# Kernel optimization log

Measured on AMD Instinct MI355X. Metric: run time of the kernel, lower is better.

## Reference

```python
import jax, jax.numpy as jnp
from jax import lax
import numpy as np
from functools import partial

B, C, H, W = 4, 3, 256, 256
HW = H * W
KCAP = 32          # max tracked components per (batch, class) slot
MAX_ITER = 5
KSIZE = 5


def _depthwise_sum(x, k):
    c = x.shape[1]
    w = jnp.ones((c, 1, k, k), x.dtype)
    return lax.conv_general_dilated(x, w, (1, 1), [(k // 2, k // 2)] * 2,
                                    feature_group_count=c,
                                    dimension_numbers=('NCHW', 'OIHW', 'NCHW'))


def erode(x):
    return (_depthwise_sum(x, KSIZE) >= KSIZE * KSIZE - 0.5).astype(x.dtype)


def dilate(x):
    return (_depthwise_sum(x, KSIZE) > 0.5).astype(x.dtype)


def _maxpool3_int(L):
    return lax.reduce_window(L, jnp.int32(0), lax.max, (1, 1, 3, 3), (1, 1, 1, 1),
                             [(0, 0), (0, 0), (1, 1), (1, 1)])


def label_cc(binary):
    # connected-component labeling by iterated 3x3 max-pool of pixel indices,
    # exactly as find_components_max_pool (labels = max flat pixel index in comp)
    b = lax.stop_gradient(binary) > 0.5
    idx = jnp.arange(HW, dtype=jnp.int32).reshape(1, 1, H, W)
    L0 = jnp.where(b, idx, 0)

    def cond(st):
        return st[1]

    def body(st):
        L, _ = st
        Ln = jnp.where(b, _maxpool3_int(L), 0)
        return Ln, jnp.any(Ln != L)

    L, _ = lax.while_loop(cond, body, (L0, jnp.array(True)))
    return L


def extract_components(Lf, binf):
    # per (b,c): top-KCAP components sorted by comp.sum() = size*label/maxL (desc)
    flat = Lf.reshape(-1)
    sizes = jnp.zeros((HW,), jnp.float32).at[flat].add(binf.reshape(-1))
    idx = jnp.arange(HW, dtype=jnp.int32)
    is_root = (flat == idx) & (flat > 0)  # label 0 excluded, as in torch code
    key = jnp.where(is_root, lax.stop_gradient(sizes) * idx.astype(jnp.float32), -1.0)
    _, top_lab = lax.top_k(key, KCAP)
    valid = key[top_lab] > 0.0
    maxL = jnp.maximum(flat.max(), 1).astype(jnp.float32)
    v = top_lab.astype(jnp.float32)
    s = jnp.where(valid, sizes[top_lab] * v / maxL, 0.0)  # comp.sum()
    lab = jnp.where(valid, top_lab, -1)
    # component tensor = mask * label/maxL, exactly mask*L/max(L) of the original
    comps = (Lf[None] == lab[:, None, None]).astype(jnp.float32) * (v / maxL)[:, None, None]
    return s, comps, valid


def process_step(P, n, bar, s, comps, valid, t):
    # overlaps vs components stored BEFORE this step; new comps within a step
    # are pixel-disjoint so they can never match each other (overlap == 0).
    OV = jnp.einsum('jhw,khw->jk', comps, P)

    def body(carry, inp):
        P, n, bar = carry
        s_j, comp_j, valid_j, ov_j = inp
        best = jnp.argmax(ov_j)
        matched = ov_j[best] > 0.0
        widx = jnp.clip(jnp.where(matched, best, n), 0, KCAP - 1)
        can = valid_j & (matched | (n < KCAP))
        bar = bar.at[widx, t].set(jnp.where(can, s_j, bar[widx, t]))
        add = valid_j & (~matched) & (n < KCAP)
        nw = jnp.minimum(n, KCAP - 1)
        P = P.at[nw].set(jnp.where(add, comp_j, P[nw]))
        return (P, n + add.astype(n.dtype), bar), None

    (P, n, bar), _ = lax.scan(body, (P, n, bar), (s, comps, valid, OV))
    return P, n, bar


def compute_barcodes(binary):
    half = MAX_ITER // 2
    seq = [(binary, half)]
    m = binary
    for t in range(half):
        m = erode(m)
        seq.append((m, half + t + 1))
    m = binary
    for t in range(half):
        m = dilate(m)
        seq.append((m, half - t - 1))
    BC = B * C
    P = jnp.zeros((BC, KCAP, H, W), jnp.float32)
    n = jnp.zeros((BC,), jnp.int32)
    bar = jnp.zeros((BC, KCAP, MAX_ITER), jnp.float32)
    for mp, t in seq:  # fixed 5-step schedule (structural loop)
        L = label_cc(mp).reshape(BC, H, W)
        s, comps, valid = jax.vmap(extract_components)(L, mp.reshape(BC, H, W))
        P, n, bar = jax.vmap(partial(process_step, t=t))(P, n, bar, s, comps, valid)
    return bar.reshape(B, C, KCAP, MAX_ITER), n.reshape(B, C)


def topo_forward(predictions, gumbel, targets):
    y_soft = jax.nn.softmax(predictions + gumbel, axis=1)
    hard = jax.nn.one_hot(jnp.argmax(y_soft, axis=1), C, axis=1, dtype=jnp.float32)
    binary_pred = hard + y_soft - lax.stop_gradient(y_soft)  # straight-through
    binary_tgt = jnp.moveaxis(jax.nn.one_hot(targets, C, dtype=jnp.float32), -1, 1)
    bp, n_p = compute_barcodes(binary_pred)
    bt, n_t = compute_barcodes(binary_tgt)
    k = jnp.arange(KCAP)
    valid_p = k[None, None] < n_p[:, :, None]
    has_t = k[None, None] < n_t[:, :, None]
    pmax = bp.max(-1)
    pmax = jnp.where(pmax > 0, pmax, 1.0)
    tgt = jnp.where(has_t[..., None], bt, 0.0)
    term = jnp.sum((tgt - bp) ** 2, -1) / pmax ** 2
    losses = jnp.sum(jnp.where(valid_p, term, 0.0), axis=(1, 2))
    return losses.mean()  # reduction='mean'


def setup_inputs() -> dict:
    key = jax.random.key(0)
    k1, k2, k3 = jax.random.split(key, 3)
    # blob-like logits: low-res noise upsampled so component counts stay < KCAP
    lo = jax.random.normal(k1, (B, C, 16, 16), jnp.float32)
    predictions = 8.0 * jax.image.resize(lo, (B, C, H, W), 'linear')
    lo_t = jax.random.normal(k2, (B, C, 16, 16), jnp.float32)
    targets = jnp.argmax(jax.image.resize(lo_t, (B, C, H, W), 'linear'), axis=1).astype(jnp.int32)
    u = jax.random.uniform(k3, (B, C, H, W), jnp.float32, minval=1e-6, maxval=1.0 - 1e-6)
    gumbel = -jnp.log(-jnp.log(u))  # standard Gumbel noise (F.gumbel_softmax)
    return {"predictions": predictions, "gumbel": gumbel, "targets": targets}


def reference(predictions, gumbel, targets):
    return topo_forward(predictions, gumbel, targets)
```

## Files before the change

### kernel.cpp

```cpp
#include <hip/hip_runtime.h>

#define NB 4
#define NC 3
#define BC 12
#define HW 65536
#define KCAP 32
#define MAXI 5
#define RUNCAP 16384
#define NSLOT 120
#define NCH 24

typedef unsigned long long u64;
typedef unsigned int u32;

__device__ __forceinline__ int uf_find(int* P, int x){
  while (true){
    int p = P[x];
    if (p == x) return x;
    int gp = P[p];
    if (gp == p) return p;
    P[x] = gp;
    x = gp;
  }
}
__device__ __forceinline__ void uf_union_max(int* P, int a, int b){
  while (true){
    a = uf_find(P, a); b = uf_find(P, b);
    if (a == b) return;
    if (a > b){ int t = a; a = b; b = t; }
    int old = atomicCAS(&P[a], a, b);
    if (old == a) return;
    a = old;
  }
}

template<typename F>
__device__ __forceinline__ void walk_runs(const u64* wv, F&& emit){
  int open_s = -1;
  #pragma unroll
  for (int wi = 0; wi < 4; wi++){
    u64 v = wv[wi];
    int base = wi << 6;
    int pos = 0;
    while (pos < 64){
      u64 rem = v >> pos;
      if (open_s >= 0){
        u64 nz = ~rem;
        int z = nz ? __builtin_ctzll(nz) : 64;
        if (z >= 64 - pos){ pos = 64; }
        else { emit(open_s, base + pos + z); open_s = -1; pos += z; }
      } else {
        if (rem == 0ull){ pos = 64; }
        else {
          int o = __builtin_ctzll(rem);
          open_s = base + pos + o;
          pos += o;
        }
      }
    }
  }
  if (open_s >= 0) emit(open_s, 256);
}

__global__ void k_bin(const float* __restrict__ pred, const float* __restrict__ gum,
                      const int* __restrict__ tgt, u64* __restrict__ bmAll){
  int g = blockIdx.x * 256 + threadIdx.x;
  int b = g >> 16, p = g & (HW - 1);
  size_t base = (size_t)b * NC * HW + p;
  float v0 = pred[base]        + gum[base];
  float v1 = pred[base + HW]   + gum[base + HW];
  float v2 = pred[base + 2*HW] + gum[base + 2*HW];
  int a = 0; float m = v0;
  if (v1 > m){ m = v1; a = 1; }
  if (v2 > m){ m = v2; a = 2; }
  int tg = tgt[(size_t)b * HW + p];
  u64 p0 = __ballot(a == 0), p1 = __ballot(a == 1), p2 = __ballot(a == 2);
  u64 t0 = __ballot(tg == 0), t1 = __ballot(tg == 1), t2 = __ballot(tg == 2);
  if ((threadIdx.x & 63) == 0){
    int w = p >> 6;
    int sp = b * NC;
    bmAll[(size_t)(sp + 0) * 1024 + w] = p0;
    bmAll[(size_t)(sp + 1) * 1024 + w] = p1;
    bmAll[(size_t)(sp + 2) * 1024 + w] = p2;
    int st = 60 + b * NC;
    bmAll[(size_t)(st + 0) * 1024 + w] = t0;
    bmAll[(size_t)(st + 1) * 1024 + w] = t1;
    bmAll[(size_t)(st + 2) * 1024 + w] = t2;
  }
}

__global__ void k_morph4(const u64* __restrict__ bmAll, u64* __restrict__ bmAllW,
                         int4 srcs, int4 dsts, int4 flgs){
  int t = blockIdx.x * 256 + threadIdx.x;
  int job = t / 12288, rest = t % 12288;
  int s = rest >> 10, word = rest & 1023;
  int row = word >> 2, w = word & 3;
  int srcG = job == 0 ? srcs.x : job == 1 ? srcs.y : job == 2 ? srcs.z : srcs.w;
  int dstG = job == 0 ? dsts.x : job == 1 ? dsts.y : job == 2 ? dsts.z : dsts.w;
  int er   = job == 0 ? flgs.x : job == 1 ? flgs.y : job == 2 ? flgs.z : flgs.w;
  const u64* bs = bmAll + (size_t)(srcG * BC + s) * 1024;
  u64 res = er ? ~0ull : 0ull;
  for (int dy = -2; dy <= 2; dy++){
    int y = row + dy;
    if (y < 0 || y > 255){ if (er) res = 0; continue; }
    const u64* rw = bs + y * 4;
    u64 m = rw[w];
    u64 l = (w > 0) ? rw[w-1] : 0ull;
    u64 r = (w < 3) ? rw[w+1] : 0ull;
    u64 x1l = (m << 1) | (l >> 63);
    u64 x2l = (m << 2) | (l >> 62);
    u64 x1r = (m >> 1) | (r << 63);
    u64 x2r = (m >> 2) | (r << 62);
    u64 h = er ? (m & x1l & x2l & x1r & x2r) : (m | x1l | x2l | x1r | x2r);
    res = er ? (res & h) : (res | h);
  }
  bmAllW[(size_t)(dstG * BC + s) * 1024 + word] = res;
}

__global__ __launch_bounds__(1024) void k_cc_runs(
    const u64* __restrict__ bmAll, u32* __restrict__ selRuns,
    int* __restrict__ selCnt, float* __restrict__ sSel, float* __restrict__ scaleSel){
  __shared__ int par[RUNCAP];
  __shared__ u32 pkz[RUNCAP];
  __shared__ int rs[257];
  __shared__ u64 wcand[16*KCAP];
  __shared__ u64 selKeys[KCAP];
  __shared__ int selRoot[KCAP];
  __shared__ int wsum[4], wsum2[4];
  __shared__ int lmS;
  int u = blockIdx.x, t = threadIdx.x;
  int lane = t & 63, wid = t >> 6;
  bool rowT = t < 256;
  u64 wv[4] = {0,0,0,0};
  int nr = 0;
  if (rowT){
    const u64* bp = bmAll + (size_t)u * 1024 + t * 4;
    #pragma unroll
    for (int i = 0; i < 4; i++) wv[i] = bp[i];
    walk_runs(wv, [&](int a, int b){ (void)a; (void)b; nr++; });
  }
  if (t == 0) lmS = 0;
  {
    int v = nr;
    #pragma unroll
    for (int d = 1; d < 64; d <<= 1){
      int o = __shfl_up(v, d);
      if (lane >= d) v += o;
    }
    if (rowT && lane == 63) wsum[wid] = v;
    __syncthreads();
    if (rowT){
      int pre = 0;
      for (int q = 0; q < wid; q++) pre += wsum[q];
      rs[t] = pre + v - nr;
      if (t == 255) rs[256] = pre + v;
    }
    __syncthreads();
  }
  int NR = rs[256];
  int NRc = NR < RUNCAP ? NR : RUNCAP;
  int myBase = rowT ? rs[t] : 0;
  for (int i = t; i < NRc; i += 1024) par[i] = i;
  if (rowT){
    int o = myBase;
    walk_runs(wv, [&](int a, int b){
      if (o < RUNCAP) pkz[o] = ((u32)t << 16) | ((u32)a << 8) | (u32)(b - 1);
      o++;
    });
  }
  __syncthreads();
  for (int i = t; i < NRc; i += 1024){
    u32 v = pkz[i];
    int r = v >> 16;
    if (r == 0) continue;
    int s2 = (int)((v >> 8) & 255), E2 = (int)(v & 255);
    int a0 = rs[r-1], a1 = rs[r];
    if (a1 > NRc) a1 = NRc;
    if (a0 >= a1) continue;
    int lo = a0, hi = a1;
    while (lo < hi){
      int mid = (lo + hi) >> 1;
      if ((int)(pkz[mid] & 255) >= s2 - 1) hi = mid; else lo = mid + 1;
    }
    for (int j = lo; j < a1; j++){
      int s1 = (int)((pkz[j] >> 8) & 255);
      if (s1 > E2 + 1) break;
      uf_union_max(par, i, j);
    }
  }
  __syncthreads();
  for (int i = t; i < NRc; i += 1024){
    int r = i, p = par[r];
    while (p != r){ r = p; p = par[r]; }
    par[i] = r;
  }
  __syncthreads();
  {
    int lm = 0;
    for (int i0 = 0; i0 < NRc; i0 += 1024){
      int i = i0 + t;
      int root = -1, len = 0;
      if (i < NRc){
        u32 v = pkz[i];
        int s0 = (int)((v >> 8) & 255), E = (int)(v & 255);
        len = E - s0 + 1;
        root = par[i] & 16383;
        lm = max(lm, (int)(v >> 16) * 256 + E);
      }
      int val = len;
      int prev = __shfl_up(root, 1);
      unsigned flg = (lane == 0 || prev != root) ? 1u : 0u;
      #pragma unroll
      for (int d = 1; d < 64; d <<= 1){
        int ov = __shfl_up(val, d);
        unsigned of = __shfl_up(flg, d);
        if (lane >= d){
          if (!flg) val += ov;
          flg |= of;
        }
      }
      int nroot = __shfl_down(root, 1);
      bool last = (lane == 63) || (nroot != root);
      if (i < NRc && last) atomicAdd(&par[root], val << 14);
    }
    #pragma unroll
    for (int off = 32; off > 0; off >>= 1) lm = max(lm, __shfl_xor(lm, off));
    if (lane == 0) atomicMax(&lmS, lm);
  }
  __syncthreads();
  float maxLf = (float)(lmS >= 1 ? lmS : 1);
  for (int i = t; i < NRc; i += 1024){
    int pv = par[i];
    if ((pv & 16383) == i){
      u32 v = pkz[i];
      int lab = (int)(v >> 16) * 256 + (int)(v & 255);
      if (lab > 0){
        float key = (float)((u32)pv >> 14) * (float)lab;
        pkz[i] = __float_as_uint(key);
        par[i] = (lab << 14) | i;
      } else {
        pkz[i] = 0;
      }
    }
  }
  __syncthreads();
  {
    u64 myBest = 0;
    for (int i = t; i < NRc; i += 1024){
      int pv = par[i];
      if ((pv & 16383) != i) continue;
      u32 kh = pkz[i];
      if (!kh) continue;
      u64 cand = ((u64)kh << 32) | ((u64)(0xFFFFu - ((u32)pv >> 14)) << 16) | (u64)i;
      if (cand > myBest) myBest = cand;
    }
    if (lane < KCAP) wcand[wid*KCAP + lane] = 0;
    for (int r = 0; r < KCAP; r++){
      u64 b = myBest;
      #pragma unroll
      for (int off = 32; off > 0; off >>= 1){
        u64 o = __shfl_xor(b, off);
        b = (o > b) ? o : b;
      }
      if (b == 0) break;
      if (lane == 0) wcand[wid*KCAP + r] = b;
      if (myBest == b){
        pkz[(int)(b & 16383)] = 0;
        myBest = 0;
        for (int i = t; i < NRc; i += 1024){
          int pv = par[i];
          if ((pv & 16383) != i) continue;
          u32 kh = pkz[i];
          if (!kh) continue;
          u64 cand = ((u64)kh << 32) | ((u64)(0xFFFFu - ((u32)pv >> 14)) << 16) | (u64)i;
          if (cand > myBest) myBest = cand;
        }
      }
    }
  }
  __syncthreads();
  if (wid == 0){
    u64 c[8];
    #pragma unroll
    for (int q = 0; q < 8; q++) c[q] = wcand[q*64 + lane];
    if (lane < KCAP) selKeys[lane] = 0;
    for (int r = 0; r < KCAP; r++){
      u64 b = 0;
      #pragma unroll
      for (int q = 0; q < 8; q++) b = (c[q] > b) ? c[q] : b;
      #pragma unroll
      for (int off = 32; off > 0; off >>= 1){
        u64 o = __shfl_xor(b, off);
        b = (o > b) ? o : b;
      }
      if (b == 0) break;
      #pragma unroll
      for (int q = 0; q < 8; q++) if (c[q] == b) c[q] = 0;
      if (lane == 0) selKeys[r] = b;
    }
  }
  __syncthreads();
  if (t < KCAP){
    u64 k = selKeys[t];
    if (k){
      int lab = 0xFFFF - (int)((k >> 16) & 0xFFFF);
      selRoot[t] = (int)(k & 0x3FFF);
      sSel[u*KCAP + t]     = __uint_as_float((u32)(k >> 32)) / maxLf;
      scaleSel[u*KCAP + t] = (float)lab / maxLf;
    } else {
      selRoot[t] = -1;
      sSel[u*KCAP + t] = 0.0f;
      scaleSel[u*KCAP + t] = 0.0f;
    }
  }
  __syncthreads();
  for (int i = t; i < NRc; i += 1024) pkz[i] = 255u;
  __syncthreads();
  if (t < KCAP && selRoot[t] >= 0) pkz[selRoot[t]] = (u32)t;
  __syncthreads();
  int c = 0;
  if (rowT){
    int o = myBase;
    walk_runs(wv, [&](int a, int b){
      if (o < RUNCAP && pkz[par[o] & 16383] < KCAP) c++;
      o++;
    });
  }
  {
    int v = c;
    #pragma unroll
    for (int d = 1; d < 64; d <<= 1){
      int o = __shfl_up(v, d);
      if (lane >= d) v += o;
    }
    if (rowT && lane == 63) wsum2[wid] = v;
    __syncthreads();
    if (rowT){
      int pre = 0;
      for (int q = 0; q < wid; q++) pre += wsum2[q];
      int w = pre + v - c;
      size_t base = (size_t)u * RUNCAP;
      int o = myBase;
      walk_runs(wv, [&](int a, int b){
        if (o < RUNCAP){
          u32 j = pkz[par[o] & 16383];
          if (j < KCAP){
            selRuns[base + w] = (j << 24) | ((u32)t << 16) | ((u32)a << 8) | (u32)(b - 1);
            w++;
          }
        }
        o++;
      });
    }
    if (t == 0) selCnt[u] = wsum2[0] + wsum2[1] + wsum2[2] + wsum2[3];
  }
}

__global__ __launch_bounds__(1024, 4) void k_chainall(
    const u32* __restrict__ selRuns, const int* __restrict__ selCnt,
    const float* __restrict__ sSel, const float* __restrict__ scaleSel,
    float* __restrict__ barP, float* __restrict__ barT,
    int* __restrict__ n24, u64* __restrict__ PbT){
  int w = blockIdx.x, t = threadIdx.x;
  int pass = w / 12, s = w % 12;
  __shared__ u64 shbuf[8192];
  __shared__ float spL[KCAP];
  __shared__ int add_dst[KCAP];
  __shared__ int bestA[KCAP];
  __shared__ float bvA[KCAP];
  __shared__ int nS;
  int* cnt = (int*)shbuf;
  if (t < KCAP) spL[t] = 0.0f;
  if (t == 0) nS = 0;
  float* bar = (pass ? barT : barP) + (size_t)s * KCAP * MAXI;
  u64* Pb = PbT + (size_t)w * KCAP * 1024;
  int g = t >> 5, k = t & 31;
  int wid = t >> 6;
  int cw = wid * KCAP * KCAP;
  #pragma unroll 1
  for (int st = 0; st < 5; st++){
    int u = (pass * 5 + st) * BC + s;
    int tval = (st < 3) ? st + 2 : (st == 3 ? 1 : 0);
    for (int i = t; i < 16*KCAP*KCAP; i += 1024) cnt[i] = 0;
    __syncthreads();
    int n0 = nS;
    int NS = selCnt[u];
    const u32* rp = selRuns + (size_t)u * RUNCAP;
    #define OVRUN(vv, jj, aacc) { \
      jj = (int)((vv) >> 24); aacc = 0; \
      if (jj < KCAP && k < n0){ \
        int row_ = ((vv) >> 16) & 255, s0_ = ((vv) >> 8) & 255, E_ = (int)((vv) & 255); \
        int w0_ = s0_ >> 6, w1_ = E_ >> 6; \
        for (int wi_ = w0_; wi_ <= w1_; wi_++){ \
          int lo_ = max(s0_, wi_ << 6), hi_ = min(E_ + 1, (wi_ << 6) + 64); \
          u64 m_ = (hi_ - lo_ == 64) ? ~0ull : ((((u64)1 << (hi_ - lo_)) - 1) << (lo_ - (wi_ << 6))); \
          aacc += __popcll(Pb[(size_t)(row_ * 4 + wi_) * KCAP + k] & m_); \
        } \
      } }
    if (n0 > 0){
      for (int i = g; i < NS; i += 128){
        u32 va = rp[i];
        u32 vb = (i + 32 < NS) ? rp[i + 32] : 0xFFFFFFFFu;
        u32 vc = (i + 64 < NS) ? rp[i + 64] : 0xFFFFFFFFu;
        u32 vd = (i + 96 < NS) ? rp[i + 96] : 0xFFFFFFFFu;
        int j0, j1, j2, j3, a0, a1, a2, a3;
        OVRUN(va, j0, a0);
        OVRUN(vb, j1, a1);
        OVRUN(vc, j2, a2);
        OVRUN(vd, j3, a3);
        if (a0) atomicAdd(&cnt[cw + j0*KCAP + k], a0);
        if (a1) atomicAdd(&cnt[cw + j1*KCAP + k], a1);
        if (a2) atomicAdd(&cnt[cw + j2*KCAP + k], a2);
        if (a3) atomicAdd(&cnt[cw + j3*KCAP + k], a3);
      }
    }
    #undef OVRUN
    __syncthreads();
    {
      int tot = 0;
      #pragma unroll
      for (int wq = 0; wq < 16; wq++) tot += cnt[wq*KCAP*KCAP + t];
      __syncthreads();
      cnt[t] = tot;
    }
    __syncthreads();
    if (t < KCAP){
      float sn = scaleSel[(size_t)u*KCAP + t];
      int best = 0; float bv = 0.0f;
      if (sn > 0.0f && n0 > 0){
        bv = sn * spL[0] * (float)cnt[t*KCAP + 0];
        for (int k2 = 1; k2 < n0; k2++){
          float ov = sn * spL[k2] * (float)cnt[t*KCAP + k2];
          if (ov > bv){ bv = ov; best = k2; }
        }
      }
      bestA[t] = best; bvA[t] = bv;
    }
    __syncthreads();
    if (t == 0){
      int n = n0;
      for (int j = 0; j < KCAP; j++){
        add_dst[j] = -1;
        float sv = scaleSel[(size_t)u*KCAP + j];
        if (sv <= 0.0f) continue;
        if (bvA[j] > 0.0f){
          bar[bestA[j]*MAXI + tval] = sSel[(size_t)u*KCAP + j];
        } else if (n < KCAP){
          bar[n*MAXI + tval] = sSel[(size_t)u*KCAP + j];
          spL[n] = sv;
          add_dst[j] = n;
          n++;
        }
      }
      nS = n;
    }
    __syncthreads();
    int nTot = nS;
    for (int b0 = n0; b0 < nTot; b0 += 8){
      int bcnt = min(8, nTot - b0);
      for (int x = t; x < 8192; x += 1024) shbuf[x] = 0ull;
      __syncthreads();
      for (int i = t; i < NS; i += 1024){
        u32 v = rp[i];
        int j = v >> 24;
        if (j >= KCAP) continue;
        int d = add_dst[j];
        if (d < b0 || d >= b0 + bcnt) continue;
        int row = (v >> 16) & 255, s0 = (v >> 8) & 255, E = (int)(v & 255);
        int w0 = s0 >> 6, w1 = E >> 6;
        for (int wi = w0; wi <= w1; wi++){
          int lo = max(s0, wi << 6), hi = min(E + 1, (wi << 6) + 64);
          u64 mask = (hi - lo == 64) ? ~0ull : ((((u64)1 << (hi - lo)) - 1) << (lo - (wi << 6)));
          atomicOr(&shbuf[(size_t)(row * 4 + wi) * 8 + (d - b0)], mask);
        }
      }
      __syncthreads();
      for (int dd = 0; dd < bcnt; dd++)
        Pb[(size_t)t * KCAP + b0 + dd] = shbuf[(size_t)t * 8 + dd];
      __syncthreads();
    }
    __syncthreads();
  }
  if (t == 0) n24[w] = nS;
}

__global__ void k_loss(const float* __restrict__ barP, const float* __restrict__ barT,
                       const int* __restrict__ n24, float* __restrict__ out){
  __shared__ float red[512];
  int t = threadIdx.x;
  float val = 0.0f;
  if (t < BC * KCAP){
    int s = t >> 5, k = t & 31;
    int np = n24[s], nt = n24[12 + s];
    if (k < np){
      const float* bp = barP + (size_t)(s*KCAP + k)*MAXI;
      float pmax = bp[0];
      #pragma unroll
      for (int q = 1; q < MAXI; q++) pmax = fmaxf(pmax, bp[q]);
      if (!(pmax > 0.0f)) pmax = 1.0f;
      float acc = 0.0f;
      #pragma unroll
      for (int q = 0; q < MAXI; q++){
        float tv = (k < nt) ? barT[(size_t)(s*KCAP + k)*MAXI + q] : 0.0f;
        float d = tv - bp[q];
        acc += d * d;
      }
      val = acc / (pmax * pmax);
    }
  }
  red[t] = val;
  __syncthreads();
  for (int off = 256; off > 0; off >>= 1){
    if (t < off) red[t] += red[t + off];
    __syncthreads();
  }
  if (t == 0) out[0] = red[0] * 0.25f;
}

extern "C" void kernel_launch(void* const* d_in, const int* in_sizes, int n_in,
                              void* d_out, int out_size, void* d_ws, size_t ws_size,
                              hipStream_t stream){
  const float* pred = (const float*)d_in[0];
  const float* gum  = (const float*)d_in[1];
  const int*   tgt  = (const int*)d_in[2];
  float* out = (float*)d_out;
  char* ws = (char*)d_ws;
  size_t off = 0;
  auto alloc = [&](size_t bytes)->char*{
    char* p = ws + off;
    off += (bytes + 255) & ~(size_t)255;
    return p;
  };
  u64* bmAll   = (u64*)alloc((size_t)NSLOT*1024*8);
  u32* selRuns = (u32*)alloc((size_t)NSLOT*RUNCAP*4);
  int* selCnt  = (int*)alloc(NSLOT*4);
  float* sSel     = (float*)alloc((size_t)NSLOT*KCAP*4);
  float* scaleSel = (float*)alloc((size_t)NSLOT*KCAP*4);
  u64* PbT     = (u64*)alloc((size_t)NCH*KCAP*1024*8);
  int* n24     = (int*)alloc(NCH*4);
  size_t zbytes = (size_t)(BC*KCAP*MAXI*2)*4;
  char* zreg = alloc(zbytes);
  float* barP = (float*)zreg;
  float* barT = barP + BC*KCAP*MAXI;
  if (off > ws_size) return;

  hipMemsetAsync(zreg, 0, zbytes, stream);
  k_bin<<<(NB*HW)/256,256,0,stream>>>(pred, gum, tgt, bmAll);
  k_morph4<<<192,256,0,stream>>>(bmAll, bmAll, make_int4(0,0,5,5), make_int4(1,3,6,8), make_int4(1,0,1,0));
  k_morph4<<<192,256,0,stream>>>(bmAll, bmAll, make_int4(1,3,6,8), make_int4(2,4,7,9), make_int4(1,0,1,0));
  k_cc_runs<<<NSLOT,1024,0,stream>>>(bmAll, selRuns, selCnt, sSel, scaleSel);
  k_chainall<<<NCH,1024,0,stream>>>(selRuns, selCnt, sSel, scaleSel, barP, barT, n24, PbT);
  k_loss<<<1,512,0,stream>>>(barP, barT, n24, out);
}
```

Before: 271.0 us.

## Split run-union into per-wave row bands then cross-band seam pass

Union-find merging of row runs is split into two phases. First, each wavefront handles the runs in its own 16-row band, so unions stay mostly local to one wave and contend less on shared parent entries. A second pass after a barrier merges only the runs on band-boundary rows with the row above. This adds one block barrier and can leave load imbalance across waves when run counts per band differ.

```diff
diff --git a/kernel.cpp b/kernel.cpp
--- a/kernel.cpp
+++ b/kernel.cpp
@@ -169,25 +169,42 @@
     });
   }
   __syncthreads();
+  #define SEAM_EDGES(i) { \
+    u32 v_ = pkz[i]; \
+    int r_ = v_ >> 16; \
+    int s2_ = (int)((v_ >> 8) & 255), E2_ = (int)(v_ & 255); \
+    int a0_ = rs[r_-1], a1_ = rs[r_]; \
+    if (a1_ > NRc) a1_ = NRc; \
+    if (a0_ < a1_){ \
+      int lo_ = a0_, hi_ = a1_; \
+      while (lo_ < hi_){ \
+        int mid_ = (lo_ + hi_) >> 1; \
+        if ((int)(pkz[mid_] & 255) >= s2_ - 1) hi_ = mid_; else lo_ = mid_ + 1; \
+      } \
+      for (int j_ = lo_; j_ < a1_; j_++){ \
+        int s1_ = (int)((pkz[j_] >> 8) & 255); \
+        if (s1_ > E2_ + 1) break; \
+        uf_union_max(par, i, j_); \
+      } \
+    } }
+  {
+    int rLo = wid << 4;
+    int iBeg = rs[rLo], iEnd = rs[rLo + 16];
+    if (iBeg > NRc) iBeg = NRc;
+    if (iEnd > NRc) iEnd = NRc;
+    for (int i = iBeg + lane; i < iEnd; i += 64){
+      int r = (int)(pkz[i] >> 16);
+      if ((r & 15) == 0) continue;
+      SEAM_EDGES(i);
+    }
+  }
+  __syncthreads();
   for (int i = t; i < NRc; i += 1024){
-    u32 v = pkz[i];
-    int r = v >> 16;
-    if (r == 0) continue;
-    int s2 = (int)((v >> 8) & 255), E2 = (int)(v & 255);
-    int a0 = rs[r-1], a1 = rs[r];
-    if (a1 > NRc) a1 = NRc;
-    if (a0 >= a1) continue;
-    int lo = a0, hi = a1;
-    while (lo < hi){
-      int mid = (lo + hi) >> 1;
-      if ((int)(pkz[mid] & 255) >= s2 - 1) hi = mid; else lo = mid + 1;
-    }
-    for (int j = lo; j < a1; j++){
-      int s1 = (int)((pkz[j] >> 8) & 255);
-      if (s1 > E2 + 1) break;
-      uf_union_max(par, i, j);
-    }
-  }
+    int r = (int)(pkz[i] >> 16);
+    if (r == 0 || (r & 15) != 0) continue;
+    SEAM_EDGES(i);
+  }
+  #undef SEAM_EDGES
   __syncthreads();
   for (int i = t; i < NRc; i += 1024){
     int r = i, p = par[r];
```

New measurement: 288.0 us. 6.3% more time.
